# Kernel tuning notes

Measured on AMD Instinct MI355X. Metric: run time of the kernel, lower is better.

## Reference

```python
import jax, jax.numpy as jnp
import numpy as np

B, D, H = 4096, 1024, 1024

def _glorot(key, shape):
    fan_in, fan_out = shape
    limit = np.sqrt(6.0 / (fan_in + fan_out))
    return jax.random.uniform(key, shape, jnp.float32, -limit, limit)

def setup_inputs() -> dict:
    key = jax.random.key(0)
    ks = jax.random.split(key, 12)
    inp = {
        'inputs': jax.random.normal(ks[0], (B, D), jnp.float32),
        'h_prev': jax.random.normal(ks[1], (B, H), jnp.float32),
        'c_prev': jax.random.normal(ks[2], (B, H), jnp.float32),
    }
    names = ['f', 'i', 'c', 'o']
    for j, n in enumerate(names):
        inp['W_' + n] = _glorot(ks[3 + 2 * j], (D, H))
        inp['U_' + n] = _glorot(ks[4 + 2 * j], (H, H))
        inp['b_' + n] = jnp.zeros((H,), jnp.float32)
    return inp

def reference(inputs, h_prev, c_prev, W_f, U_f, b_f, W_i, U_i, b_i, W_c, U_c, b_c, W_o, U_o, b_o):
    f_t = jax.nn.sigmoid(inputs @ W_f + h_prev @ U_f + b_f)
    i_t = jax.nn.sigmoid(inputs @ W_i + h_prev @ U_i + b_i)
    c_tilde = jnp.tanh(inputs @ W_c + h_prev @ U_c + b_c)
    c_next = f_t * c_prev + i_t * c_tilde
    o_t = jax.nn.sigmoid(inputs @ W_o + h_prev @ U_o + b_o)
    h_next = o_t * jnp.tanh(c_next)
    return (h_next, c_next)
```

## Files before the change

### kernel.cpp

```cpp
#include <hip/hip_runtime.h>


typedef __attribute__((ext_vector_type(8))) short bfrag8;

__device__ __forceinline__ unsigned int f2bf(float f) {
  unsigned int u = __builtin_bit_cast(unsigned int, f);
  unsigned int r = (u + 0x7fffu + ((u >> 16) & 1u)) >> 16;
  return r & 0xffffu;
}

__global__ __launch_bounds__(256) void prep_x(const float* __restrict__ inputs,
                                              const float* __restrict__ h_prev,
                                              unsigned short* __restrict__ X) {
  int idx = blockIdx.x * 256 + threadIdx.x;
  int b  = idx >> 8;
  int k8 = (idx & 255) * 8;
  const float* src = (k8 < 1024) ? (inputs + (size_t)b * 1024 + k8)
                                 : (h_prev + (size_t)b * 1024 + (k8 - 1024));
  float4 v0 = ((const float4*)src)[0];
  float4 v1 = ((const float4*)src)[1];
  uint4 o;
  o.x = f2bf(v0.x) | (f2bf(v0.y) << 16);
  o.y = f2bf(v0.z) | (f2bf(v0.w) << 16);
  o.z = f2bf(v1.x) | (f2bf(v1.y) << 16);
  o.w = f2bf(v1.z) | (f2bf(v1.w) << 16);
  *(uint4*)(X + (size_t)b * 2048 + k8) = o;
}

__global__ __launch_bounds__(256) void prep_w(
    const float* __restrict__ s0, const float* __restrict__ s1,
    const float* __restrict__ s2, const float* __restrict__ s3,
    const float* __restrict__ s4, const float* __restrict__ s5,
    const float* __restrict__ s6, const float* __restrict__ s7,
    unsigned short* __restrict__ Wct) {
  int blk = blockIdx.x;
  int m = blk >> 8;
  const float* src = (m == 0) ? s0 : (m == 1) ? s1 : (m == 2) ? s2 : (m == 3) ? s3
                   : (m == 4) ? s4 : (m == 5) ? s5 : (m == 6) ? s6 : s7;
  int g = m >> 1, half = m & 1;
  unsigned short* dst = Wct + (size_t)g * 1024 * 2048 + (size_t)half * 1024;
  int t = blk & 255;
  int k0 = (t >> 4) * 64;
  int h0 = (t & 15) * 64;
  __shared__ float lt[64][68];
  int tid = threadIdx.x;
  #pragma unroll
  for (int it = 0; it < 4; ++it) {
    int r  = (tid >> 4) + it * 16;
    int c4 = (tid & 15) * 4;
    float4 v = *(const float4*)(src + (size_t)(k0 + r) * 1024 + h0 + c4);
    lt[r][c4 + 0] = v.x; lt[r][c4 + 1] = v.y; lt[r][c4 + 2] = v.z; lt[r][c4 + 3] = v.w;
  }
  __syncthreads();
  #pragma unroll
  for (int it = 0; it < 4; ++it) {
    int hh  = (tid >> 4) + it * 16;
    int kk4 = (tid & 15) * 4;
    uint2 o;
    o.x = f2bf(lt[kk4 + 0][hh]) | (f2bf(lt[kk4 + 1][hh]) << 16);
    o.y = f2bf(lt[kk4 + 2][hh]) | (f2bf(lt[kk4 + 3][hh]) << 16);
    *(uint2*)(dst + (size_t)(h0 + hh) * 2048 + k0 + kk4) = o;
  }
}


#define FENCE() asm volatile("" ::: "memory")
#define BARRIER() do { FENCE(); __builtin_amdgcn_s_barrier(); FENCE(); } while (0)
#define VMCNT(n) asm volatile("s_waitcnt vmcnt(" #n ")" ::: "memory")
#define LGKM(n) asm volatile("s_waitcnt lgkmcnt(" #n ")" ::: "memory")
#define GLOAD16(gp, lp) __builtin_amdgcn_global_load_lds( \
    (const __attribute__((address_space(1))) unsigned int*)(gp), \
    (__attribute__((address_space(3))) unsigned int*)(lp), 16, 0, 0)
#define DSR(dst, addr, off) asm volatile("ds_read_b128 %0, %1 offset:%c2" \
    : "=v"(dst) : "v"(addr), "n"(off))

#define AC "a0","a1","a2","a3","a4","a5","a6","a7","a8","a9","a10","a11","a12","a13","a14","a15", \
 "a16","a17","a18","a19","a20","a21","a22","a23","a24","a25","a26","a27","a28","a29","a30","a31", \
 "a32","a33","a34","a35","a36","a37","a38","a39","a40","a41","a42","a43","a44","a45","a46","a47", \
 "a48","a49","a50","a51","a52","a53","a54","a55","a56","a57","a58","a59","a60","a61","a62","a63", \
 "a64","a65","a66","a67","a68","a69","a70","a71","a72","a73","a74","a75","a76","a77","a78","a79", \
 "a80","a81","a82","a83","a84","a85","a86","a87","a88","a89","a90","a91","a92","a93","a94","a95", \
 "a96","a97","a98","a99","a100","a101","a102","a103","a104","a105","a106","a107","a108","a109","a110","a111", \
 "a112","a113","a114","a115","a116","a117","a118","a119","a120","a121","a122","a123","a124","a125","a126","a127"

#define WZ(n) "v_accvgpr_write_b32 a" #n ", 0\n\t"
#define AINIT() asm volatile( \
 WZ(0)WZ(1)WZ(2)WZ(3)WZ(4)WZ(5)WZ(6)WZ(7)WZ(8)WZ(9)WZ(10)WZ(11)WZ(12)WZ(13)WZ(14)WZ(15) \
 WZ(16)WZ(17)WZ(18)WZ(19)WZ(20)WZ(21)WZ(22)WZ(23)WZ(24)WZ(25)WZ(26)WZ(27)WZ(28)WZ(29)WZ(30)WZ(31) \
 WZ(32)WZ(33)WZ(34)WZ(35)WZ(36)WZ(37)WZ(38)WZ(39)WZ(40)WZ(41)WZ(42)WZ(43)WZ(44)WZ(45)WZ(46)WZ(47) \
 WZ(48)WZ(49)WZ(50)WZ(51)WZ(52)WZ(53)WZ(54)WZ(55)WZ(56)WZ(57)WZ(58)WZ(59)WZ(60)WZ(61)WZ(62)WZ(63) \
 WZ(64)WZ(65)WZ(66)WZ(67)WZ(68)WZ(69)WZ(70)WZ(71)WZ(72)WZ(73)WZ(74)WZ(75)WZ(76)WZ(77)WZ(78)WZ(79) \
 WZ(80)WZ(81)WZ(82)WZ(83)WZ(84)WZ(85)WZ(86)WZ(87)WZ(88)WZ(89)WZ(90)WZ(91)WZ(92)WZ(93)WZ(94)WZ(95) \
 WZ(96)WZ(97)WZ(98)WZ(99)WZ(100)WZ(101)WZ(102)WZ(103)WZ(104)WZ(105)WZ(106)WZ(107)WZ(108)WZ(109)WZ(110)WZ(111) \
 WZ(112)WZ(113)WZ(114)WZ(115)WZ(116)WZ(117)WZ(118)WZ(119)WZ(120)WZ(121)WZ(122)WZ(123)WZ(124)WZ(125)WZ(126)WZ(127) \
 ::: AC)

#define MFMA_ONE(BR, AF, BF) asm volatile( \
    "v_mfma_f32_16x16x32_bf16 a[" BR "], %0, %1, a[" BR "]" \
    :: "v"(AF), "v"(BF) : AC)

#define CLUSTER16(A4, B4, R00,R01,R02,R03, R10,R11,R12,R13, R20,R21,R22,R23, R30,R31,R32,R33) do { \
  __builtin_amdgcn_s_setprio(1); \
  MFMA_ONE(R00, (A4)[0], (B4)[0]); MFMA_ONE(R01, (A4)[1], (B4)[0]); \
  MFMA_ONE(R02, (A4)[2], (B4)[0]); MFMA_ONE(R03, (A4)[3], (B4)[0]); \
  MFMA_ONE(R10, (A4)[0], (B4)[1]); MFMA_ONE(R11, (A4)[1], (B4)[1]); \
  MFMA_ONE(R12, (A4)[2], (B4)[1]); MFMA_ONE(R13, (A4)[3], (B4)[1]); \
  MFMA_ONE(R20, (A4)[0], (B4)[2]); MFMA_ONE(R21, (A4)[1], (B4)[2]); \
  MFMA_ONE(R22, (A4)[2], (B4)[2]); MFMA_ONE(R23, (A4)[3], (B4)[2]); \
  MFMA_ONE(R30, (A4)[0], (B4)[3]); MFMA_ONE(R31, (A4)[1], (B4)[3]); \
  MFMA_ONE(R32, (A4)[2], (B4)[3]); MFMA_ONE(R33, (A4)[3], (B4)[3]); \
  __builtin_amdgcn_s_setprio(0); \
} while (0)

#define CL_MH0(A4, B4) CLUSTER16(A4, B4, \
  "0:3","4:7","8:11","12:15", "32:35","36:39","40:43","44:47", \
  "64:67","68:71","72:75","76:79", "96:99","100:103","104:107","108:111")
#define CL_MH1(A4, B4) CLUSTER16(A4, B4, \
  "16:19","20:23","24:27","28:31", "48:51","52:55","56:59","60:63", \
  "80:83","84:87","88:91","92:95", "112:115","116:119","120:123","124:127")

#define READ_A4(arr, BUF, MH, ABASE) do { \
  DSR(arr[0], ABASE, (BUF)*32768 + (MH)*8192 + 0);    \
  DSR(arr[1], ABASE, (BUF)*32768 + (MH)*8192 + 2048); \
  DSR(arr[2], ABASE, (BUF)*32768 + (MH)*8192 + 4096); \
  DSR(arr[3], ABASE, (BUF)*32768 + (MH)*8192 + 6144); \
} while (0)

#define READ_B4N(arr, BUF, BBASE) do { \
  DSR(arr[0], BBASE, (BUF)*32768 + 0);    \
  DSR(arr[1], BBASE, (BUF)*32768 + 2048); \
  DSR(arr[2], BBASE, (BUF)*32768 + 4096); \
  DSR(arr[3], BBASE, (BUF)*32768 + 6144); \
} while (0)

#define STAGE_A(BUF, H, kt) do { int _kb = ((kt) < 32 ? (kt) : 31) * 64; \
  GLOAD16(pA0 + (size_t)(H) * 262144 + _kb, smem + (BUF)*32768 + (H)*16384 + stbase); \
  GLOAD16(pA1 + (size_t)(H) * 262144 + _kb, smem + (BUF)*32768 + (H)*16384 + stbase + 1024); \
} while (0)

#define STAGE_B(BUF, kt) do { int _kb = ((kt) < 32 ? (kt) : 31) * 64; \
  GLOAD16(pB00 + _kb, smem + 65536 + (BUF)*32768 + stbase); \
  GLOAD16(pB01 + _kb, smem + 65536 + (BUF)*32768 + stbase + 1024); \
  GLOAD16(pB10 + _kb, smem + 65536 + (BUF)*32768 + 16384 + stbase); \
  GLOAD16(pB11 + _kb, smem + 65536 + (BUF)*32768 + 16384 + stbase + 1024); \
} while (0)

#define ARD(X, RS) asm volatile("v_accvgpr_read_b32 %0, " RS : "=v"(X))

#define EPI_M(Mi, F0,F1,F2,F3, I0,I1,I2,I3, C0,C1,C2,C3, O0,O1,O2,O3) do { \
  float pf[4], pi[4], pc[4], po[4]; \
  ARD(pf[0],F0); ARD(pf[1],F1); ARD(pf[2],F2); ARD(pf[3],F3); \
  ARD(pi[0],I0); ARD(pi[1],I1); ARD(pi[2],I2); ARD(pi[3],I3); \
  ARD(pc[0],C0); ARD(pc[1],C1); ARD(pc[2],C2); ARD(pc[3],C3); \
  ARD(po[0],O0); ARD(po[1],O1); ARD(po[2],O2); ARD(po[3],O3); \
  _Pragma("unroll") for (int j = 0; j < 4; ++j) { \
    const int b = rbw + (Mi) * 16 + q * 4 + j; \
    float xf = pf[j] + Bgf, xi = pi[j] + Bgi, xc = pc[j] + Bgc, xo = po[j] + Bgo; \
    float fg = 1.f / (1.f + __expf(-xf)); \
    float ig = 1.f / (1.f + __expf(-xi)); \
    float ct = 2.f / (1.f + __expf(-2.f * xc)) - 1.f; \
    float og = 1.f / (1.f + __expf(-xo)); \
    float cn = fg * c_prev[(size_t)b * 1024 + hcol] + ig * ct; \
    float hn = og * (2.f / (1.f + __expf(-2.f * cn)) - 1.f); \
    out[(size_t)b * 1024 + hcol] = hn; \
    out[(size_t)4194304 + (size_t)b * 1024 + hcol] = cn; \
  } \
} while (0)

__global__ __launch_bounds__(512, 2) void lstm_gemm(
    const unsigned short* __restrict__ X, const unsigned short* __restrict__ Wct,
    const float* __restrict__ c_prev,
    const float* __restrict__ bfv, const float* __restrict__ biv,
    const float* __restrict__ bcv, const float* __restrict__ bov,
    float* __restrict__ out) {
  extern __shared__ __align__(16) char smem[];
  const int tid = threadIdx.x;
  const int lane = tid & 63, w = tid >> 6;
  const int u = lane & 15, q = (lane >> 4) & 3;
  const int wm = w >> 2, wn = w & 3;

  const int bid = blockIdx.x;
  const int xcd = bid & 7, idx = bid >> 3;
  const int row0 = (idx & 15) * 256;
  const int h0 = (xcd * 2 + (idx >> 4)) * 64;

  const unsigned lds0 = (unsigned)(size_t)((__attribute__((address_space(3))) char*)smem);

  const int sw0 = (q ^ (u & 7)) << 4;
  const int sw1 = ((q + 4) ^ (u & 7)) << 4;
  const unsigned aA0 = lds0 + wm * 16384 + u * 128 + sw0;
  const unsigned aA1 = lds0 + wm * 16384 + u * 128 + sw1;
  const unsigned aB0 = lds0 + 65536 + (wn * 64 + u) * 128 + sw0;
  const unsigned aB1 = lds0 + 65536 + (wn * 64 + u) * 128 + sw1;

  const int stbase = w * 2048 + lane * 16;
  const int rA0 = w * 16 + (lane >> 3), rA1 = rA0 + 8;
  const int ssA = (lane & 7) ^ (rA0 & 7);
  const unsigned short* pA0 = X + (size_t)(row0 + rA0) * 2048 + ssA * 8;
  const unsigned short* pA1 = X + (size_t)(row0 + rA1) * 2048 + ssA * 8;
  auto wrow = [&](int C) { return (((C >> 4) & 3) << 10) + h0 + ((C >> 6) << 4) + (C & 15); };
  const unsigned short* pB00 = Wct + (size_t)wrow(rA0) * 2048 + ssA * 8;
  const unsigned short* pB01 = Wct + (size_t)wrow(rA1) * 2048 + ssA * 8;
  const unsigned short* pB10 = Wct + (size_t)wrow(128 + rA0) * 2048 + ssA * 8;
  const unsigned short* pB11 = Wct + (size_t)wrow(128 + rA1) * 2048 + ssA * 8;

  AINIT();

  bfrag8 Ab0[4], Ab1[4], Bb0[4], Bb1[4];

  STAGE_A(0, 0, 0); STAGE_A(0, 1, 0);
  STAGE_B(0, 0);
  STAGE_B(1, 1);
  VMCNT(4);
  BARRIER();
  READ_A4(Ab0, 0, 0, aA0);
  READ_B4N(Bb0, 0, aB0);

  #pragma unroll 1
  for (int t = 0; t < 16; ++t) {
    const int kt1 = 2 * t + 1, kt2 = 2 * t + 2, kt3 = 2 * t + 3;
    READ_A4(Ab1, 0, 1, aA0);
    STAGE_A(1, 0, kt1); STAGE_A(1, 1, kt1);
    BARRIER(); LGKM(4);
    CL_MH0(Ab0, Bb0);
    READ_A4(Ab0, 0, 0, aA1);
    READ_B4N(Bb1, 0, aB1);
    BARRIER(); LGKM(8);
    CL_MH1(Ab1, Bb0);
    READ_A4(Ab1, 0, 1, aA1);
    VMCNT(0);
    BARRIER(); LGKM(4);
    CL_MH0(Ab0, Bb1);
    READ_A4(Ab0, 1, 0, aA0);
    READ_B4N(Bb0, 1, aB0);
    STAGE_B(0, kt2);
    BARRIER(); LGKM(8);
    CL_MH1(Ab1, Bb1);
    READ_A4(Ab1, 1, 1, aA0);
    STAGE_A(0, 0, kt2); STAGE_A(0, 1, kt2);
    BARRIER(); LGKM(4);
    CL_MH0(Ab0, Bb0);
    READ_A4(Ab0, 1, 0, aA1);
    READ_B4N(Bb1, 1, aB1);
    BARRIER(); LGKM(8);
    CL_MH1(Ab1, Bb0);
    READ_A4(Ab1, 1, 1, aA1);
    VMCNT(0);
    BARRIER(); LGKM(4);
    CL_MH0(Ab0, Bb1);
    READ_A4(Ab0, 0, 0, aA0);
    READ_B4N(Bb0, 0, aB0);
    STAGE_B(1, kt3);
    BARRIER(); LGKM(8);
    CL_MH1(Ab1, Bb1);
  }
  VMCNT(0); LGKM(0);
  asm volatile("s_nop 7\n\ts_nop 7");

  const int hcol = h0 + wn * 16 + u;
  const float Bgf = bfv[hcol], Bgi = biv[hcol], Bgc = bcv[hcol], Bgo = bov[hcol];
  const int rbw = row0 + wm * 128;
  EPI_M(0, "a0","a1","a2","a3",     "a32","a33","a34","a35",
           "a64","a65","a66","a67", "a96","a97","a98","a99");
  EPI_M(1, "a4","a5","a6","a7",     "a36","a37","a38","a39",
           "a68","a69","a70","a71", "a100","a101","a102","a103");
  EPI_M(2, "a8","a9","a10","a11",   "a40","a41","a42","a43",
           "a72","a73","a74","a75", "a104","a105","a106","a107");
  EPI_M(3, "a12","a13","a14","a15", "a44","a45","a46","a47",
           "a76","a77","a78","a79", "a108","a109","a110","a111");
  EPI_M(4, "a16","a17","a18","a19", "a48","a49","a50","a51",
           "a80","a81","a82","a83", "a112","a113","a114","a115");
  EPI_M(5, "a20","a21","a22","a23", "a52","a53","a54","a55",
           "a84","a85","a86","a87", "a116","a117","a118","a119");
  EPI_M(6, "a24","a25","a26","a27", "a56","a57","a58","a59",
           "a88","a89","a90","a91", "a120","a121","a122","a123");
  EPI_M(7, "a28","a29","a30","a31", "a60","a61","a62","a63",
           "a92","a93","a94","a95", "a124","a125","a126","a127");
}

extern "C" void kernel_launch(void* const* d_in, const int* in_sizes, int n_in,
                              void* d_out, int out_size, void* d_ws, size_t ws_size,
                              hipStream_t stream) {
  const float* inputs = (const float*)d_in[0];
  const float* h_prev = (const float*)d_in[1];
  const float* c_prev = (const float*)d_in[2];
  const float* Wf = (const float*)d_in[3];
  const float* Uf = (const float*)d_in[4];
  const float* bf = (const float*)d_in[5];
  const float* Wi = (const float*)d_in[6];
  const float* Ui = (const float*)d_in[7];
  const float* bi = (const float*)d_in[8];
  const float* Wc = (const float*)d_in[9];
  const float* Uc = (const float*)d_in[10];
  const float* bc = (const float*)d_in[11];
  const float* Wo = (const float*)d_in[12];
  const float* Uo = (const float*)d_in[13];
  const float* bo = (const float*)d_in[14];
  float* out = (float*)d_out;

  unsigned short* X   = (unsigned short*)d_ws;
  unsigned short* Wct = X + (size_t)4096 * 2048;

  (void)hipFuncSetAttribute(reinterpret_cast<const void*>(lstm_gemm),
                            hipFuncAttributeMaxDynamicSharedMemorySize, 131072);

  prep_x<<<4096, 256, 0, stream>>>(inputs, h_prev, X);
  prep_w<<<2048, 256, 0, stream>>>(Wf, Uf, Wi, Ui, Wc, Uc, Wo, Uo, Wct);
  lstm_gemm<<<256, 512, 131072, stream>>>(X, Wct, c_prev, bf, bi, bc, bo, out);
}
```

Before: 87.29 us.

## Switch GEMM inner loop from 16x16x32 to 32x32x16 bf16 MFMA tiles

Replaces the sixteen 16x16x32 MFMAs per cluster with eight 32x32x16 MFMAs, which changes the LDS read addressing (per-k-slice swizzled base pointers) and the accumulator register layout. The epilogue is rewritten to pull 16-register accumulator blocks and uses cross-lane shuffles to regroup the four gate values per output element before the LSTM nonlinearities. The goal is fewer MFMA issues and fewer LDS fragment reads per unit of work, since larger tiles reuse each fragment more. In exchange the epilogue gains shuffle traffic and the fragment-to-gate mapping gets more complex and riskier to get right.

```diff
diff --git a/kernel.cpp b/kernel.cpp
--- a/kernel.cpp
+++ b/kernel.cpp
@@ -95,42 +95,34 @@
  WZ(112)WZ(113)WZ(114)WZ(115)WZ(116)WZ(117)WZ(118)WZ(119)WZ(120)WZ(121)WZ(122)WZ(123)WZ(124)WZ(125)WZ(126)WZ(127) \
  ::: AC)
 
-#define MFMA_ONE(BR, AF, BF) asm volatile( \
-    "v_mfma_f32_16x16x32_bf16 a[" BR "], %0, %1, a[" BR "]" \
+#define M32(BR, AF, BF) asm volatile( \
+    "v_mfma_f32_32x32x16_bf16 a[" BR "], %0, %1, a[" BR "]" \
     :: "v"(AF), "v"(BF) : AC)
 
-#define CLUSTER16(A4, B4, R00,R01,R02,R03, R10,R11,R12,R13, R20,R21,R22,R23, R30,R31,R32,R33) do { \
+#define CL8(A4, B4, T00, T01, T10, T11) do { \
   __builtin_amdgcn_s_setprio(1); \
-  MFMA_ONE(R00, (A4)[0], (B4)[0]); MFMA_ONE(R01, (A4)[1], (B4)[0]); \
-  MFMA_ONE(R02, (A4)[2], (B4)[0]); MFMA_ONE(R03, (A4)[3], (B4)[0]); \
-  MFMA_ONE(R10, (A4)[0], (B4)[1]); MFMA_ONE(R11, (A4)[1], (B4)[1]); \
-  MFMA_ONE(R12, (A4)[2], (B4)[1]); MFMA_ONE(R13, (A4)[3], (B4)[1]); \
-  MFMA_ONE(R20, (A4)[0], (B4)[2]); MFMA_ONE(R21, (A4)[1], (B4)[2]); \
-  MFMA_ONE(R22, (A4)[2], (B4)[2]); MFMA_ONE(R23, (A4)[3], (B4)[2]); \
-  MFMA_ONE(R30, (A4)[0], (B4)[3]); MFMA_ONE(R31, (A4)[1], (B4)[3]); \
-  MFMA_ONE(R32, (A4)[2], (B4)[3]); MFMA_ONE(R33, (A4)[3], (B4)[3]); \
+  M32(T00, (A4)[0], (B4)[0]); M32(T01, (A4)[2], (B4)[0]); \
+  M32(T10, (A4)[0], (B4)[2]); M32(T11, (A4)[2], (B4)[2]); \
+  M32(T00, (A4)[1], (B4)[1]); M32(T01, (A4)[3], (B4)[1]); \
+  M32(T10, (A4)[1], (B4)[3]); M32(T11, (A4)[3], (B4)[3]); \
   __builtin_amdgcn_s_setprio(0); \
 } while (0)
 
-#define CL_MH0(A4, B4) CLUSTER16(A4, B4, \
-  "0:3","4:7","8:11","12:15", "32:35","36:39","40:43","44:47", \
-  "64:67","68:71","72:75","76:79", "96:99","100:103","104:107","108:111")
-#define CL_MH1(A4, B4) CLUSTER16(A4, B4, \
-  "16:19","20:23","24:27","28:31", "48:51","52:55","56:59","60:63", \
-  "80:83","84:87","88:91","92:95", "112:115","116:119","120:123","124:127")
-
-#define READ_A4(arr, BUF, MH, ABASE) do { \
-  DSR(arr[0], ABASE, (BUF)*32768 + (MH)*8192 + 0);    \
-  DSR(arr[1], ABASE, (BUF)*32768 + (MH)*8192 + 2048); \
-  DSR(arr[2], ABASE, (BUF)*32768 + (MH)*8192 + 4096); \
-  DSR(arr[3], ABASE, (BUF)*32768 + (MH)*8192 + 6144); \
-} while (0)
-
-#define READ_B4N(arr, BUF, BBASE) do { \
-  DSR(arr[0], BBASE, (BUF)*32768 + 0);    \
-  DSR(arr[1], BBASE, (BUF)*32768 + 2048); \
-  DSR(arr[2], BBASE, (BUF)*32768 + 4096); \
-  DSR(arr[3], BBASE, (BUF)*32768 + 6144); \
+#define CL_MH0(A4, B4) CL8(A4, B4, "0:15",  "16:31", "64:79",  "80:95")
+#define CL_MH1(A4, B4) CL8(A4, B4, "32:47", "48:63", "96:111", "112:127")
+
+#define READ_A4(arr, BUF, MH, KH) do { \
+  DSR(arr[0], vA[2*(KH)+0], (BUF)*32768 + ((MH)*2+0)*4096); \
+  DSR(arr[1], vA[2*(KH)+1], (BUF)*32768 + ((MH)*2+0)*4096); \
+  DSR(arr[2], vA[2*(KH)+0], (BUF)*32768 + ((MH)*2+1)*4096); \
+  DSR(arr[3], vA[2*(KH)+1], (BUF)*32768 + ((MH)*2+1)*4096); \
+} while (0)
+
+#define READ_B4(arr, BUF, KH) do { \
+  DSR(arr[0], vB[2*(KH)+0], (BUF)*32768 + 0);    \
+  DSR(arr[1], vB[2*(KH)+1], (BUF)*32768 + 0);    \
+  DSR(arr[2], vB[2*(KH)+0], (BUF)*32768 + 4096); \
+  DSR(arr[3], vB[2*(KH)+1], (BUF)*32768 + 4096); \
 } while (0)
 
 #define STAGE_A(BUF, H, kt) do { int _kb = ((kt) < 32 ? (kt) : 31) * 64; \
@@ -147,19 +139,40 @@
 
 #define ARD(X, RS) asm volatile("v_accvgpr_read_b32 %0, " RS : "=v"(X))
 
-#define EPI_M(Mi, F0,F1,F2,F3, I0,I1,I2,I3, C0,C1,C2,C3, O0,O1,O2,O3) do { \
-  float pf[4], pi[4], pc[4], po[4]; \
-  ARD(pf[0],F0); ARD(pf[1],F1); ARD(pf[2],F2); ARD(pf[3],F3); \
-  ARD(pi[0],I0); ARD(pi[1],I1); ARD(pi[2],I2); ARD(pi[3],I3); \
-  ARD(pc[0],C0); ARD(pc[1],C1); ARD(pc[2],C2); ARD(pc[3],C3); \
-  ARD(po[0],O0); ARD(po[1],O1); ARD(po[2],O2); ARD(po[3],O3); \
-  _Pragma("unroll") for (int j = 0; j < 4; ++j) { \
-    const int b = rbw + (Mi) * 16 + q * 4 + j; \
-    float xf = pf[j] + Bgf, xi = pi[j] + Bgi, xc = pc[j] + Bgc, xo = po[j] + Bgo; \
-    float fg = 1.f / (1.f + __expf(-xf)); \
-    float ig = 1.f / (1.f + __expf(-xi)); \
-    float ct = 2.f / (1.f + __expf(-2.f * xc)) - 1.f; \
-    float og = 1.f / (1.f + __expf(-xo)); \
+#define ARD16(arr, N0,N1,N2,N3,N4,N5,N6,N7,N8,N9,NA,NB,NC,ND,NE,NF) do { \
+  ARD(arr[0],N0); ARD(arr[1],N1); ARD(arr[2],N2); ARD(arr[3],N3); \
+  ARD(arr[4],N4); ARD(arr[5],N5); ARD(arr[6],N6); ARD(arr[7],N7); \
+  ARD(arr[8],N8); ARD(arr[9],N9); ARD(arr[10],NA); ARD(arr[11],NB); \
+  ARD(arr[12],NC); ARD(arr[13],ND); ARD(arr[14],NE); ARD(arr[15],NF); \
+} while (0)
+
+#define EPI_MT(MT) do { \
+  float o0[16], o1[16], r0[8], r1[8]; \
+  if ((MT) == 0) { ARD16(o0,"a0","a1","a2","a3","a4","a5","a6","a7","a8","a9","a10","a11","a12","a13","a14","a15"); \
+                   ARD16(o1,"a64","a65","a66","a67","a68","a69","a70","a71","a72","a73","a74","a75","a76","a77","a78","a79"); } \
+  if ((MT) == 1) { ARD16(o0,"a16","a17","a18","a19","a20","a21","a22","a23","a24","a25","a26","a27","a28","a29","a30","a31"); \
+                   ARD16(o1,"a80","a81","a82","a83","a84","a85","a86","a87","a88","a89","a90","a91","a92","a93","a94","a95"); } \
+  if ((MT) == 2) { ARD16(o0,"a32","a33","a34","a35","a36","a37","a38","a39","a40","a41","a42","a43","a44","a45","a46","a47"); \
+                   ARD16(o1,"a96","a97","a98","a99","a100","a101","a102","a103","a104","a105","a106","a107","a108","a109","a110","a111"); } \
+  if ((MT) == 3) { ARD16(o0,"a48","a49","a50","a51","a52","a53","a54","a55","a56","a57","a58","a59","a60","a61","a62","a63"); \
+                   ARD16(o1,"a112","a113","a114","a115","a116","a117","a118","a119","a120","a121","a122","a123","a124","a125","a126","a127"); } \
+  _Pragma("unroll") for (int k = 0; k < 8; ++k) { \
+    float s0 = g1 ? o0[k] : o0[k + 8];    \
+    float s1 = g1 ? o1[k] : o1[k + 8]; \
+    r0[k] = __shfl_xor(s0, 16, 64); \
+    r1[k] = __shfl_xor(s1, 16, 64); \
+  } \
+  _Pragma("unroll") for (int k = 0; k < 8; ++k) { \
+    float pf = g1 ? r0[k] : o0[k]; \
+    float pi = g1 ? o0[k + 8] : r0[k]; \
+    float pc = g1 ? r1[k] : o1[k]; \
+    float po = g1 ? o1[k + 8] : r1[k]; \
+    const int b = rbw + (MT) * 32 + (k & 3) + 8 * (k >> 2); \
+    pf += Bgf; pi += Bgi; pc += Bgc; po += Bgo; \
+    float fg = 1.f / (1.f + __expf(-pf)); \
+    float ig = 1.f / (1.f + __expf(-pi)); \
+    float ct = 2.f / (1.f + __expf(-2.f * pc)) - 1.f; \
+    float og = 1.f / (1.f + __expf(-po)); \
     float cn = fg * c_prev[(size_t)b * 1024 + hcol] + ig * ct; \
     float hn = og * (2.f / (1.f + __expf(-2.f * cn)) - 1.f); \
     out[(size_t)b * 1024 + hcol] = hn; \
@@ -176,8 +189,9 @@
   extern __shared__ __align__(16) char smem[];
   const int tid = threadIdx.x;
   const int lane = tid & 63, w = tid >> 6;
-  const int u = lane & 15, q = (lane >> 4) & 3;
   const int wm = w >> 2, wn = w & 3;
+  const int l31 = lane & 31, l7 = lane & 7, h5 = lane >> 5;
+  const int g1 = (lane >> 4) & 1;
 
   const int bid = blockIdx.x;
   const int xcd = bid & 7, idx = bid >> 3;
@@ -186,12 +200,17 @@
 
   const unsigned lds0 = (unsigned)(size_t)((__attribute__((address_space(3))) char*)smem);
 
-  const int sw0 = (q ^ (u & 7)) << 4;
-  const int sw1 = ((q + 4) ^ (u & 7)) << 4;
-  const unsigned aA0 = lds0 + wm * 16384 + u * 128 + sw0;
-  const unsigned aA1 = lds0 + wm * 16384 + u * 128 + sw1;
-  const unsigned aB0 = lds0 + 65536 + (wn * 64 + u) * 128 + sw0;
-  const unsigned aB1 = lds0 + 65536 + (wn * 64 + u) * 128 + sw1;
+  unsigned vA[4], vB[4];
+  {
+    const unsigned aArow = lds0 + (unsigned)(wm * 128 + l31) * 128;
+    const unsigned aBrow = lds0 + 65536 + (unsigned)(wn * 64 + l31) * 128;
+    #pragma unroll
+    for (int ks = 0; ks < 4; ++ks) {
+      const unsigned sw = (unsigned)(((2 * ks + h5) ^ l7) << 4);
+      vA[ks] = aArow + sw;
+      vB[ks] = aBrow + sw;
+    }
+  }
 
   const int stbase = w * 2048 + lane * 16;
   const int rA0 = w * 16 + (lane >> 3), rA1 = rA0 + 8;
@@ -213,69 +232,57 @@
   STAGE_B(1, 1);
   VMCNT(4);
   BARRIER();
-  READ_A4(Ab0, 0, 0, aA0);
-  READ_B4N(Bb0, 0, aB0);
+  READ_A4(Ab0, 0, 0, 0);
+  READ_B4(Bb0, 0, 0);
 
   #pragma unroll 1
   for (int t = 0; t < 16; ++t) {
     const int kt1 = 2 * t + 1, kt2 = 2 * t + 2, kt3 = 2 * t + 3;
-    READ_A4(Ab1, 0, 1, aA0);
+    READ_A4(Ab1, 0, 1, 0);
     STAGE_A(1, 0, kt1); STAGE_A(1, 1, kt1);
     BARRIER(); LGKM(4);
     CL_MH0(Ab0, Bb0);
-    READ_A4(Ab0, 0, 0, aA1);
-    READ_B4N(Bb1, 0, aB1);
+    READ_A4(Ab0, 0, 0, 1);
+    READ_B4(Bb1, 0, 1);
     BARRIER(); LGKM(8);
     CL_MH1(Ab1, Bb0);
-    READ_A4(Ab1, 0, 1, aA1);
+    READ_A4(Ab1, 0, 1, 1);
     VMCNT(0);
     BARRIER(); LGKM(4);
     CL_MH0(Ab0, Bb1);
-    READ_A4(Ab0, 1, 0, aA0);
-    READ_B4N(Bb0, 1, aB0);
+    READ_A4(Ab0, 1, 0, 0);
+    READ_B4(Bb0, 1, 0);
     STAGE_B(0, kt2);
     BARRIER(); LGKM(8);
     CL_MH1(Ab1, Bb1);
-    READ_A4(Ab1, 1, 1, aA0);
+    READ_A4(Ab1, 1, 1, 0);
     STAGE_A(0, 0, kt2); STAGE_A(0, 1, kt2);
     BARRIER(); LGKM(4);
     CL_MH0(Ab0, Bb0);
-    READ_A4(Ab0, 1, 0, aA1);
-    READ_B4N(Bb1, 1, aB1);
+    READ_A4(Ab0, 1, 0, 1);
+    READ_B4(Bb1, 1, 1);
     BARRIER(); LGKM(8);
     CL_MH1(Ab1, Bb0);
-    READ_A4(Ab1, 1, 1, aA1);
+    READ_A4(Ab1, 1, 1, 1);
     VMCNT(0);
     BARRIER(); LGKM(4);
     CL_MH0(Ab0, Bb1);
-    READ_A4(Ab0, 0, 0, aA0);
-    READ_B4N(Bb0, 0, aB0);
+    READ_A4(Ab0, 0, 0, 0);
+    READ_B4(Bb0, 0, 0);
     STAGE_B(1, kt3);
     BARRIER(); LGKM(8);
     CL_MH1(Ab1, Bb1);
   }
   VMCNT(0); LGKM(0);
-  asm volatile("s_nop 7\n\ts_nop 7");
-
-  const int hcol = h0 + wn * 16 + u;
+  asm volatile("s_nop 7\n\ts_nop 7\n\ts_nop 7");
+
+  const int hcol = h0 + wn * 16 + (lane & 15);
   const float Bgf = bfv[hcol], Bgi = biv[hcol], Bgc = bcv[hcol], Bgo = bov[hcol];
-  const int rbw = row0 + wm * 128;
-  EPI_M(0, "a0","a1","a2","a3",     "a32","a33","a34","a35",
-           "a64","a65","a66","a67", "a96","a97","a98","a99");
-  EPI_M(1, "a4","a5","a6","a7",     "a36","a37","a38","a39",
-           "a68","a69","a70","a71", "a100","a101","a102","a103");
-  EPI_M(2, "a8","a9","a10","a11",   "a40","a41","a42","a43",
-           "a72","a73","a74","a75", "a104","a105","a106","a107");
-  EPI_M(3, "a12","a13","a14","a15", "a44","a45","a46","a47",
-           "a76","a77","a78","a79", "a108","a109","a110","a111");
-  EPI_M(4, "a16","a17","a18","a19", "a48","a49","a50","a51",
-           "a80","a81","a82","a83", "a112","a113","a114","a115");
-  EPI_M(5, "a20","a21","a22","a23", "a52","a53","a54","a55",
-           "a84","a85","a86","a87", "a116","a117","a118","a119");
-  EPI_M(6, "a24","a25","a26","a27", "a56","a57","a58","a59",
-           "a88","a89","a90","a91", "a120","a121","a122","a123");
-  EPI_M(7, "a28","a29","a30","a31", "a60","a61","a62","a63",
-           "a92","a93","a94","a95", "a124","a125","a126","a127");
+  const int rbw = row0 + wm * 128 + 16 * g1 + 4 * h5;
+  EPI_MT(0);
+  EPI_MT(1);
+  EPI_MT(2);
+  EPI_MT(3);
 }
 
 extern "C" void kernel_launch(void* const* d_in, const int* in_sizes, int n_in,
```

Measured after the change: 94.29 us. 8.0% more time.
